# Optimization experiments

Hardware: AMD Instinct MI355X
Metric: run time of the kernel (lower is better)

## Reference

```python
import jax, jax.numpy as jnp
import numpy as np

NEG_INF = -1e9  # finite stand-in for Constants.NEG_INF to keep softmax NaN-free


def setup_inputs() -> dict:
    key = jax.random.key(0)
    ks = jax.random.split(key, 6)
    B, Lq, Lk, D = 32, 1024, 1024, 1024
    query = jax.random.normal(ks[0], (B, Lq, D), dtype=jnp.float32)
    context = jax.random.normal(ks[1], (B, Lk, D), dtype=jnp.float32)
    ql = jax.random.randint(ks[2], (B,), 1, Lq + 1).astype(jnp.int32)
    cl = jax.random.randint(ks[3], (B,), 1, Lk + 1).astype(jnp.int32)
    # pad_packed_sequence pads to the max length in batch -> force max present
    ql = ql.at[0].set(Lq)
    cl = cl.at[0].set(Lk)
    W_in = jax.random.normal(ks[4], (D, D), dtype=jnp.float32) * (D ** -0.5)
    W_out = jax.random.normal(ks[5], (D, 2 * D), dtype=jnp.float32) * ((2 * D) ** -0.5)
    return {"query": query, "context": context, "query_lengths": ql,
            "context_lengths": cl, "W_in": W_in, "W_out": W_out}


def reference(query, context, query_lengths, context_lengths, W_in, W_out):
    B, Lq, D = query.shape
    Lk = context.shape[1]
    # attention_type == 'general': project queries
    q = jnp.einsum('bqd,ed->bqe', query, W_in)                      # [B,Lq,D]
    scores = jnp.einsum('bqd,bkd->bqk', q, context)                 # [B,Lq,Lk]
    # pack/pad round-trips == length mask on both query and context axes
    qmask = jnp.arange(Lq)[None, :] < query_lengths[:, None]        # [B,Lq]
    kmask = jnp.arange(Lk)[None, :] < context_lengths[:, None]      # [B,Lk]
    mask = qmask[:, :, None] & kmask[:, None, :]                    # [B,Lq,Lk]
    scores_m = jnp.where(mask, scores, NEG_INF)
    weights = jax.nn.softmax(scores_m, axis=2)
    mix = jnp.einsum('bqk,bkd->bqd', weights, context)              # [B,Lq,D]
    combined = jnp.concatenate([mix, q], axis=2)                    # [B,Lq,2D]
    output = jnp.tanh(jnp.einsum('bqc,dc->bqd', combined, W_out))   # [B,Lq,D]
    return output, scores_m
```

## Files before the change

kernel.cpp:

```cpp
#include <hip/hip_runtime.h>
#include <math.h>

#define BM 128
#define BN 128
#define BK 32
#define KP 40

typedef __bf16 bf16x8 __attribute__((ext_vector_type(8)));
typedef float  floatx4 __attribute__((ext_vector_type(4)));

__device__ __forceinline__ unsigned short f2bf(float x) {
    unsigned int u = __float_as_uint(x);
    u += 0x7FFFu + ((u >> 16) & 1u);
    return (unsigned short)(u >> 16);
}
__device__ __forceinline__ float bf2f(unsigned short h) {
    return __uint_as_float(((unsigned int)h) << 16);
}

template <bool LO>
__device__ __forceinline__ void cvt_store(unsigned short* H, unsigned short* L,
                                          int idx, float4 v) {
    unsigned short h0 = f2bf(v.x), h1 = f2bf(v.y), h2 = f2bf(v.z), h3 = f2bf(v.w);
    *(ushort4*)(H + idx) = make_ushort4(h0, h1, h2, h3);
    if (LO) {
        unsigned short l0 = f2bf(v.x - bf2f(h0)), l1 = f2bf(v.y - bf2f(h1));
        unsigned short l2 = f2bf(v.z - bf2f(h2)), l3 = f2bf(v.w - bf2f(h3));
        *(ushort4*)(L + idx) = make_ushort4(l0, l1, l2, l3);
    }
}

template <int EPI, bool SOFTA, bool SPLITA, bool TRANSB, int NPASS>
__global__ __launch_bounds__(256, 2) void mfma_gemm(
    const float* __restrict__ A, const float* __restrict__ A2,
    const float* __restrict__ B, float* __restrict__ C,
    int K, int lda, int ldb, int ldc,
    long long aBatch, long long bBatch, long long cBatch,
    const float2* __restrict__ stats, long long statsBatch,
    const int* __restrict__ qlen, const int* __restrict__ klen)
{
    constexpr bool PIPE = (NPASS == 1);

    const int b = blockIdx.z;
    A += aBatch * b;
    B += bBatch * b;
    C += cBatch * b;

    __shared__ __align__(16) unsigned short smem[(BM + BN) * KP * 2];
    unsigned short* Ah = smem;
    unsigned short* Al = Ah + BM * KP;
    unsigned short* Bh = Al + BM * KP;
    unsigned short* Bl = Bh + BN * KP;
    float* Bt = (float*)Bh;

    const int tid = threadIdx.x;
    const int m0 = blockIdx.y * BM;
    const int n0 = blockIdx.x * BN;

    const int sr = tid >> 3;
    const int sc = (tid & 7) << 2;

    const int wv = tid >> 6;
    const int wm = (wv >> 1) << 6;
    const int wn = (wv & 1) << 6;
    const int lane = tid & 63;
    const int lm = lane & 15;
    const int lk = (lane >> 4) << 3;

    floatx4 acc[4][4];
#pragma unroll
    for (int i = 0; i < 4; i++)
#pragma unroll
        for (int j = 0; j < 4; j++) acc[i][j] = (floatx4)0.f;

    float2 st[4];
    if (SOFTA) {
        const float2* sp = stats + statsBatch * b;
#pragma unroll
        for (int r = 0; r < 4; r++) st[r] = sp[m0 + (r << 5) + sr];
    }

    auto ldA = [&](int k0, float4* va) {
        const float* Ap = A;
        int kk = k0;
        if (SPLITA) {
            const int half = K >> 1;
            Ap = (k0 < half) ? A : A2;
            kk = k0 & (half - 1);
        }
#pragma unroll
        for (int r = 0; r < 4; r++) {
            const int row = (r << 5) + sr;
            va[r] = *(const float4*)(Ap + (size_t)(m0 + row) * lda + kk + sc);
        }
    };
    auto ldB = [&](int k0, float4* vb) {
        if (!TRANSB) {
#pragma unroll
            for (int r = 0; r < 4; r++) {
                const int row = (r << 5) + sr;
                vb[r] = *(const float4*)(B + (size_t)(n0 + row) * ldb + k0 + sc);
            }
        } else {
            const int kr = tid >> 3;
            const int c4 = (tid & 7) << 2;
#pragma unroll
            for (int r = 0; r < 4; r++) {
                const int col = (r << 5) + c4;
                const float* src = B + (size_t)(k0 + kr) * ldb + n0 + col;
                float2 v0 = *(const float2*)(src);
                float2 v1 = *(const float2*)(src + 2);
                vb[r] = make_float4(v0.x, v0.y, v1.x, v1.y);
            }
        }
    };
    auto stA = [&](const float4* va) {
#pragma unroll
        for (int r = 0; r < 4; r++) {
            float4 v = va[r];
            if (SOFTA) {
                v.x = expf(v.x - st[r].x) * st[r].y;
                v.y = expf(v.y - st[r].x) * st[r].y;
                v.z = expf(v.z - st[r].x) * st[r].y;
                v.w = expf(v.w - st[r].x) * st[r].y;
            }
            cvt_store<NPASS == 3>(Ah, Al, ((r << 5) + sr) * KP + sc, v);
        }
    };
    auto stB = [&](const float4* vb) {
        if (!TRANSB) {
#pragma unroll
            for (int r = 0; r < 4; r++)
                cvt_store<NPASS == 3>(Bh, Bl, ((r << 5) + sr) * KP + sc, vb[r]);
        } else {
            const int kr = tid >> 3;
            const int c4 = (tid & 7) << 2;
#pragma unroll
            for (int r = 0; r < 4; r++) {
                const int col = (r << 5) + c4;
                *(float2*)(Bt + kr * 130 + col)     = make_float2(vb[r].x, vb[r].y);
                *(float2*)(Bt + kr * 130 + col + 2) = make_float2(vb[r].z, vb[r].w);
            }
        }
    };

    float4 va[4], vb[4];
    if (PIPE) { ldA(0, va); ldB(0, vb); }

    for (int k0 = 0; k0 < K; k0 += BK) {
        if (!PIPE) { ldA(k0, va); ldB(k0, vb); }
        stA(va);
        stB(vb);
        __syncthreads();

        if (PIPE && k0 + BK < K) { ldA(k0 + BK, va); ldB(k0 + BK, vb); }

        bf16x8 ah[4], al[4], bh[4], bl[4];
#pragma unroll
        for (int t = 0; t < 4; t++) {
            const int ar = (wm + (t << 4) + lm) * KP + lk;
            ah[t] = *(const bf16x8*)(Ah + ar);
            if constexpr (NPASS == 3) al[t] = *(const bf16x8*)(Al + ar);
        }
        if (!TRANSB) {
#pragma unroll
            for (int t = 0; t < 4; t++) {
                const int br = (wn + (t << 4) + lm) * KP + lk;
                bh[t] = *(const bf16x8*)(Bh + br);
                if constexpr (NPASS == 3) bl[t] = *(const bf16x8*)(Bl + br);
            }
        } else {
#pragma unroll
            for (int t = 0; t < 4; t++) {
                const int n = wn + (t << 4) + lm;
                union { unsigned short u[8]; bf16x8 v; } th, tl;
#pragma unroll
                for (int j = 0; j < 8; j++) {
                    float x = Bt[(lk + j) * 130 + n];
                    unsigned short h = f2bf(x);
                    th.u[j] = h;
                    if constexpr (NPASS == 3) tl.u[j] = f2bf(x - bf2f(h));
                }
                bh[t] = th.v;
                if constexpr (NPASS == 3) bl[t] = tl.v;
            }
        }

#pragma unroll
        for (int i = 0; i < 4; i++)
#pragma unroll
            for (int j = 0; j < 4; j++) {
                if constexpr (NPASS == 3) {
                    acc[i][j] = __builtin_amdgcn_mfma_f32_16x16x32_bf16(al[i], bh[j], acc[i][j], 0, 0, 0);
                    acc[i][j] = __builtin_amdgcn_mfma_f32_16x16x32_bf16(ah[i], bl[j], acc[i][j], 0, 0, 0);
                }
                acc[i][j] = __builtin_amdgcn_mfma_f32_16x16x32_bf16(ah[i], bh[j], acc[i][j], 0, 0, 0);
            }
        __syncthreads();
    }

    int qb = 0, kb = 0;
    if (EPI == 1) { qb = qlen[b]; kb = klen[b]; }
    const int qd = (lane >> 4) << 2;
#pragma unroll
    for (int i = 0; i < 4; i++)
#pragma unroll
        for (int j = 0; j < 4; j++) {
            const int col = n0 + wn + (j << 4) + lm;
#pragma unroll
            for (int r = 0; r < 4; r++) {
                const int row = m0 + wm + (i << 4) + qd + r;
                float v = acc[i][j][r];
                if (EPI == 1) v = (row < qb && col < kb) ? v : -1e9f;
                else if (EPI == 2) v = tanhf(v);
                C[(size_t)row * ldc + col] = v;
            }
        }
}

__global__ __launch_bounds__(256) void row_stats_kernel(
    const float* __restrict__ S, float2* __restrict__ stats, int L)
{
    const int row = blockIdx.x * 4 + (threadIdx.x >> 6);
    const int lane = threadIdx.x & 63;
    const float* p = S + (size_t)row * L;

    float mx = -1e30f;
    for (int j = lane; j < L; j += 64) mx = fmaxf(mx, p[j]);
#pragma unroll
    for (int off = 32; off > 0; off >>= 1) mx = fmaxf(mx, __shfl_xor(mx, off, 64));

    float sm = 0.f;
    for (int j = lane; j < L; j += 64) sm += expf(p[j] - mx);
#pragma unroll
    for (int off = 32; off > 0; off >>= 1) sm += __shfl_xor(sm, off, 64);

    if (lane == 0) stats[row] = make_float2(mx, 1.f / sm);
}

extern "C" void kernel_launch(void* const* d_in, const int* in_sizes, int n_in,
                              void* d_out, int out_size, void* d_ws, size_t ws_size,
                              hipStream_t stream)
{
    const float* query   = (const float*)d_in[0];
    const float* context = (const float*)d_in[1];
    const int*   qlens   = (const int*)d_in[2];
    const int*   clens   = (const int*)d_in[3];
    const float* W_in    = (const float*)d_in[4];
    const float* W_out   = (const float*)d_in[5];

    const int B = 32, Lq = 1024, Lk = 1024, D = 1024;
    const long long nQ = (long long)B * Lq * D;

    float* out    = (float*)d_out;
    float* scores = out + nQ;

    float*  q     = (float*)d_ws;
    float*  mix   = q + nQ;
    float2* stats = (float2*)(mix + nQ);

    mfma_gemm<0, false, false, false, 3><<<dim3(D / BN, (B * Lq) / BM, 1), 256, 0, stream>>>(
        query, nullptr, W_in, q, D, D, D, D,
        0LL, 0LL, 0LL, nullptr, 0LL, nullptr, nullptr);

    mfma_gemm<1, false, false, false, 3><<<dim3(Lk / BN, Lq / BM, B), 256, 0, stream>>>(
        q, nullptr, context, scores, D, D, D, Lk,
        (long long)Lq * D, (long long)Lk * D, (long long)Lq * Lk,
        nullptr, 0LL, qlens, clens);

    row_stats_kernel<<<(B * Lq) / 4, 256, 0, stream>>>(scores, stats, Lk);

    mfma_gemm<0, true, false, true, 1><<<dim3(D / BN, Lq / BM, B), 256, 0, stream>>>(
        scores, nullptr, context, mix, Lk, Lk, D, D,
        (long long)Lq * Lk, (long long)Lk * D, (long long)Lq * D,
        stats, (long long)Lq, nullptr, nullptr);

    mfma_gemm<2, false, true, false, 1><<<dim3(D / BN, (B * Lq) / BM, 1), 256, 0, stream>>>(
        mix, q, W_out, out, 2 * D, D, 2 * D, D,
        0LL, 0LL, 0LL, nullptr, 0LL, nullptr, nullptr);
}
```

Baseline: 1.524 ms.

## Store intermediates and weights as pre-split bf16 planes, transpose-convert B into LDS

```diff
diff --git a/kernel.cpp b/kernel.cpp
--- a/kernel.cpp
+++ b/kernel.cpp
@@ -8,50 +8,56 @@
 
 typedef __bf16 bf16x8 __attribute__((ext_vector_type(8)));
 typedef float  floatx4 __attribute__((ext_vector_type(4)));
-
-__device__ __forceinline__ unsigned short f2bf(float x) {
+typedef unsigned short u16;
+
+__device__ __forceinline__ u16 f2bf(float x) {
     unsigned int u = __float_as_uint(x);
     u += 0x7FFFu + ((u >> 16) & 1u);
-    return (unsigned short)(u >> 16);
-}
-__device__ __forceinline__ float bf2f(unsigned short h) {
+    return (u16)(u >> 16);
+}
+__device__ __forceinline__ float bf2f(u16 h) {
     return __uint_as_float(((unsigned int)h) << 16);
 }
 
 template <bool LO>
-__device__ __forceinline__ void cvt_store(unsigned short* H, unsigned short* L,
-                                          int idx, float4 v) {
-    unsigned short h0 = f2bf(v.x), h1 = f2bf(v.y), h2 = f2bf(v.z), h3 = f2bf(v.w);
+__device__ __forceinline__ void cvt_store(u16* H, u16* L, int idx, float4 v) {
+    u16 h0 = f2bf(v.x), h1 = f2bf(v.y), h2 = f2bf(v.z), h3 = f2bf(v.w);
     *(ushort4*)(H + idx) = make_ushort4(h0, h1, h2, h3);
     if (LO) {
-        unsigned short l0 = f2bf(v.x - bf2f(h0)), l1 = f2bf(v.y - bf2f(h1));
-        unsigned short l2 = f2bf(v.z - bf2f(h2)), l3 = f2bf(v.w - bf2f(h3));
+        u16 l0 = f2bf(v.x - bf2f(h0)), l1 = f2bf(v.y - bf2f(h1));
+        u16 l2 = f2bf(v.z - bf2f(h2)), l3 = f2bf(v.w - bf2f(h3));
         *(ushort4*)(L + idx) = make_ushort4(l0, l1, l2, l3);
     }
 }
 
-template <int EPI, bool SOFTA, bool SPLITA, bool TRANSB, int NPASS>
+enum OpMode { OP_F32 = 0, OP_PLANES = 1, OP_BF16 = 2 };
+
+template <int EPI, bool SOFTA, bool SPLITA, bool TRANSB, int NPASS, int AMODE, int BMODE>
 __global__ __launch_bounds__(256, 2) void mfma_gemm(
-    const float* __restrict__ A, const float* __restrict__ A2,
-    const float* __restrict__ B, float* __restrict__ C,
+    const void* __restrict__ Av, const void* __restrict__ A2v,
+    const void* __restrict__ Bv, const void* __restrict__ B2v,
+    void* __restrict__ Cv, void* __restrict__ C2v,
     int K, int lda, int ldb, int ldc,
     long long aBatch, long long bBatch, long long cBatch,
     const float2* __restrict__ stats, long long statsBatch,
     const int* __restrict__ qlen, const int* __restrict__ klen)
 {
-    constexpr bool PIPE = (NPASS == 1);
-
     const int b = blockIdx.z;
-    A += aBatch * b;
-    B += bBatch * b;
-    C += cBatch * b;
-
-    __shared__ __align__(16) unsigned short smem[(BM + BN) * KP * 2];
-    unsigned short* Ah = smem;
-    unsigned short* Al = Ah + BM * KP;
-    unsigned short* Bh = Al + BM * KP;
-    unsigned short* Bl = Bh + BN * KP;
-    float* Bt = (float*)Bh;
+
+    const float* A_f  = (const float*)Av + aBatch * b;
+    const u16*   A_h  = (const u16*)Av + aBatch * b;
+    const u16*   A_l  = (const u16*)A2v + aBatch * b;
+    const u16*   A2_h = (const u16*)A2v;
+    const float* B_f  = (const float*)Bv + bBatch * b;
+    const u16*   B_h  = (const u16*)Bv + bBatch * b;
+    const u16*   B_l  = (const u16*)B2v + bBatch * b;
+
+    constexpr int LP = (NPASS == 3) ? 2 : 1;
+    __shared__ __align__(16) u16 smem[(BM + BN) * KP * LP];
+    u16* Ah = smem;
+    u16* Al = Ah + (NPASS == 3 ? BM * KP : 0);
+    u16* Bh = Ah + BM * KP * LP;
+    u16* Bl = Bh + (NPASS == 3 ? BN * KP : 0);
 
     const int tid = threadIdx.x;
     const int m0 = blockIdx.y * BM;
@@ -80,80 +86,132 @@
         for (int r = 0; r < 4; r++) st[r] = sp[m0 + (r << 5) + sr];
     }
 
-    auto ldA = [&](int k0, float4* va) {
-        const float* Ap = A;
-        int kk = k0;
-        if (SPLITA) {
-            const int half = K >> 1;
-            Ap = (k0 < half) ? A : A2;
-            kk = k0 & (half - 1);
-        }
-#pragma unroll
-        for (int r = 0; r < 4; r++) {
-            const int row = (r << 5) + sr;
-            va[r] = *(const float4*)(Ap + (size_t)(m0 + row) * lda + kk + sc);
+    float4  vaf[4]; ushort4 vah[4], vaL[4];
+    float4  vbf[4]; ushort4 vbh[4], vbL[4];
+
+    auto ldA = [&](int k0) {
+        if constexpr (AMODE == OP_F32) {
+#pragma unroll
+            for (int r = 0; r < 4; r++) {
+                const int row = (r << 5) + sr;
+                vaf[r] = *(const float4*)(A_f + (size_t)(m0 + row) * lda + k0 + sc);
+            }
+        } else if constexpr (AMODE == OP_PLANES) {
+#pragma unroll
+            for (int r = 0; r < 4; r++) {
+                const int row = (r << 5) + sr;
+                const size_t off = (size_t)(m0 + row) * lda + k0 + sc;
+                vah[r] = *(const ushort4*)(A_h + off);
+                vaL[r] = *(const ushort4*)(A_l + off);
+            }
+        } else {
+            const u16* Ap = A_h;
+            int kk = k0;
+            if constexpr (SPLITA) {
+                const int half = K >> 1;
+                Ap = (k0 < half) ? A_h : A2_h;
+                kk = k0 & (half - 1);
+            }
+#pragma unroll
+            for (int r = 0; r < 4; r++) {
+                const int row = (r << 5) + sr;
+                vah[r] = *(const ushort4*)(Ap + (size_t)(m0 + row) * lda + kk + sc);
+            }
         }
     };
-    auto ldB = [&](int k0, float4* vb) {
-        if (!TRANSB) {
-#pragma unroll
-            for (int r = 0; r < 4; r++) {
-                const int row = (r << 5) + sr;
-                vb[r] = *(const float4*)(B + (size_t)(n0 + row) * ldb + k0 + sc);
-            }
-        } else {
+    auto ldB = [&](int k0) {
+        if constexpr (TRANSB) {
             const int kr = tid >> 3;
             const int c4 = (tid & 7) << 2;
 #pragma unroll
             for (int r = 0; r < 4; r++) {
                 const int col = (r << 5) + c4;
-                const float* src = B + (size_t)(k0 + kr) * ldb + n0 + col;
+                const float* src = B_f + (size_t)(k0 + kr) * ldb + n0 + col;
                 float2 v0 = *(const float2*)(src);
                 float2 v1 = *(const float2*)(src + 2);
-                vb[r] = make_float4(v0.x, v0.y, v1.x, v1.y);
+                vbf[r] = make_float4(v0.x, v0.y, v1.x, v1.y);
+            }
+        } else if constexpr (BMODE == OP_F32) {
+#pragma unroll
+            for (int r = 0; r < 4; r++) {
+                const int row = (r << 5) + sr;
+                vbf[r] = *(const float4*)(B_f + (size_t)(n0 + row) * ldb + k0 + sc);
+            }
+        } else if constexpr (BMODE == OP_PLANES) {
+#pragma unroll
+            for (int r = 0; r < 4; r++) {
+                const int row = (r << 5) + sr;
+                const size_t off = (size_t)(n0 + row) * ldb + k0 + sc;
+                vbh[r] = *(const ushort4*)(B_h + off);
+                vbL[r] = *(const ushort4*)(B_l + off);
+            }
+        } else {
+#pragma unroll
+            for (int r = 0; r < 4; r++) {
+                const int row = (r << 5) + sr;
+                vbh[r] = *(const ushort4*)(B_h + (size_t)(n0 + row) * ldb + k0 + sc);
             }
         }
     };
-    auto stA = [&](const float4* va) {
+    auto stA = [&]() {
 #pragma unroll
         for (int r = 0; r < 4; r++) {
-            float4 v = va[r];
-            if (SOFTA) {
-                v.x = expf(v.x - st[r].x) * st[r].y;
-                v.y = expf(v.y - st[r].x) * st[r].y;
-                v.z = expf(v.z - st[r].x) * st[r].y;
-                v.w = expf(v.w - st[r].x) * st[r].y;
-            }
-            cvt_store<NPASS == 3>(Ah, Al, ((r << 5) + sr) * KP + sc, v);
+            const int idx = ((r << 5) + sr) * KP + sc;
+            if constexpr (AMODE == OP_F32) {
+                float4 v = vaf[r];
+                if (SOFTA) {
+                    v.x = expf(v.x - st[r].x) * st[r].y;
+                    v.y = expf(v.y - st[r].x) * st[r].y;
+                    v.z = expf(v.z - st[r].x) * st[r].y;
+                    v.w = expf(v.w - st[r].x) * st[r].y;
+                }
+                cvt_store<NPASS == 3>(Ah, Al, idx, v);
+            } else if constexpr (AMODE == OP_PLANES) {
+                *(ushort4*)(Ah + idx) = vah[r];
+                *(ushort4*)(Al + idx) = vaL[r];
+            } else {
+                *(ushort4*)(Ah + idx) = vah[r];
+            }
         }
     };
-    auto stB = [&](const float4* vb) {
-        if (!TRANSB) {
-#pragma unroll
-            for (int r = 0; r < 4; r++)
-                cvt_store<NPASS == 3>(Bh, Bl, ((r << 5) + sr) * KP + sc, vb[r]);
-        } else {
+    auto stB = [&]() {
+        if constexpr (TRANSB) {
             const int kr = tid >> 3;
             const int c4 = (tid & 7) << 2;
 #pragma unroll
             for (int r = 0; r < 4; r++) {
                 const int col = (r << 5) + c4;
-                *(float2*)(Bt + kr * 130 + col)     = make_float2(vb[r].x, vb[r].y);
-                *(float2*)(Bt + kr * 130 + col + 2) = make_float2(vb[r].z, vb[r].w);
+                const float4 v = vbf[r];
+                Bh[(col + 0) * KP + kr] = f2bf(v.x);
+                Bh[(col + 1) * KP + kr] = f2bf(v.y);
+                Bh[(col + 2) * KP + kr] = f2bf(v.z);
+                Bh[(col + 3) * KP + kr] = f2bf(v.w);
+            }
+        } else {
+#pragma unroll
+            for (int r = 0; r < 4; r++) {
+                const int idx = ((r << 5) + sr) * KP + sc;
+                if constexpr (BMODE == OP_F32) {
+                    cvt_store<NPASS == 3>(Bh, Bl, idx, vbf[r]);
+                } else if constexpr (BMODE == OP_PLANES) {
+                    *(ushort4*)(Bh + idx) = vbh[r];
+                    *(ushort4*)(Bl + idx) = vbL[r];
+                } else {
+                    *(ushort4*)(Bh + idx) = vbh[r];
+                }
             }
         }
     };
 
-    float4 va[4], vb[4];
-    if (PIPE) { ldA(0, va); ldB(0, vb); }
+    ldA(0);
+    ldB(0);
 
     for (int k0 = 0; k0 < K; k0 += BK) {
-        if (!PIPE) { ldA(k0, va); ldB(k0, vb); }
-        stA(va);
-        stB(vb);
+        stA();
+        stB();
         __syncthreads();
 
-        if (PIPE && k0 + BK < K) { ldA(k0 + BK, va); ldB(k0 + BK, vb); }
+        if (k0 + BK < K) { ldA(k0 + BK); ldB(k0 + BK); }
 
         bf16x8 ah[4], al[4], bh[4], bl[4];
 #pragma unroll
@@ -162,28 +220,11 @@
             ah[t] = *(const bf16x8*)(Ah + ar);
             if constexpr (NPASS == 3) al[t] = *(const bf16x8*)(Al + ar);
         }
-        if (!TRANSB) {
-#pragma unroll
-            for (int t = 0; t < 4; t++) {
-                const int br = (wn + (t << 4) + lm) * KP + lk;
-                bh[t] = *(const bf16x8*)(Bh + br);
-                if constexpr (NPASS == 3) bl[t] = *(const bf16x8*)(Bl + br);
-            }
-        } else {
-#pragma unroll
-            for (int t = 0; t < 4; t++) {
-                const int n = wn + (t << 4) + lm;
-                union { unsigned short u[8]; bf16x8 v; } th, tl;
-#pragma unroll
-                for (int j = 0; j < 8; j++) {
-                    float x = Bt[(lk + j) * 130 + n];
-                    unsigned short h = f2bf(x);
-                    th.u[j] = h;
-                    if constexpr (NPASS == 3) tl.u[j] = f2bf(x - bf2f(h));
-                }
-                bh[t] = th.v;
-                if constexpr (NPASS == 3) bl[t] = tl.v;
-            }
+#pragma unroll
+        for (int t = 0; t < 4; t++) {
+            const int br = (wn + (t << 4) + lm) * KP + lk;
+            bh[t] = *(const bf16x8*)(Bh + br);
+            if constexpr (NPASS == 3) bl[t] = *(const bf16x8*)(Bl + br);
         }
 
 #pragma unroll
@@ -199,6 +240,9 @@
         __syncthreads();
     }
 
+    float* C_f = (float*)Cv + cBatch * b;
+    u16*   C_h = (u16*)Cv + cBatch * b;
+    u16*   C_l = (u16*)C2v + cBatch * b;
     int qb = 0, kb = 0;
     if (EPI == 1) { qb = qlen[b]; kb = klen[b]; }
     const int qd = (lane >> 4) << 2;
@@ -210,10 +254,21 @@
 #pragma unroll
             for (int r = 0; r < 4; r++) {
                 const int row = m0 + wm + (i << 4) + qd + r;
+                const size_t off = (size_t)row * ldc + col;
                 float v = acc[i][j][r];
-                if (EPI == 1) v = (row < qb && col < kb) ? v : -1e9f;
-                else if (EPI == 2) v = tanhf(v);
-                C[(size_t)row * ldc + col] = v;
+                if constexpr (EPI == 0) {
+                    C_f[off] = v;
+                } else if constexpr (EPI == 1) {
+                    C_f[off] = (row < qb && col < kb) ? v : -1e9f;
+                } else if constexpr (EPI == 2) {
+                    C_f[off] = tanhf(v);
+                } else if constexpr (EPI == 3) {
+                    const u16 h = f2bf(v);
+                    C_h[off] = h;
+                    C_l[off] = f2bf(v - bf2f(h));
+                } else {
+                    C_h[off] = f2bf(v);
+                }
             }
         }
 }
@@ -236,6 +291,28 @@
     for (int off = 32; off > 0; off >>= 1) sm += __shfl_xor(sm, off, 64);
 
     if (lane == 0) stats[row] = make_float2(mx, 1.f / sm);
+}
+
+__global__ __launch_bounds__(256) void cvt_hilo_kernel(
+    const float* __restrict__ s, u16* __restrict__ hi, u16* __restrict__ lo, int n4)
+{
+    const int stride = gridDim.x * 256;
+    for (int i = blockIdx.x * 256 + threadIdx.x; i < n4; i += stride) {
+        float4 v = ((const float4*)s)[i];
+        u16 h0 = f2bf(v.x), h1 = f2bf(v.y), h2 = f2bf(v.z), h3 = f2bf(v.w);
+        ((ushort4*)hi)[i] = make_ushort4(h0, h1, h2, h3);
+        ((ushort4*)lo)[i] = make_ushort4(f2bf(v.x - bf2f(h0)), f2bf(v.y - bf2f(h1)),
+                                         f2bf(v.z - bf2f(h2)), f2bf(v.w - bf2f(h3)));
+    }
+}
+__global__ __launch_bounds__(256) void cvt_bf16_kernel(
+    const float* __restrict__ s, u16* __restrict__ d, int n4)
+{
+    const int stride = gridDim.x * 256;
+    for (int i = blockIdx.x * 256 + threadIdx.x; i < n4; i += stride) {
+        float4 v = ((const float4*)s)[i];
+        ((ushort4*)d)[i] = make_ushort4(f2bf(v.x), f2bf(v.y), f2bf(v.z), f2bf(v.w));
+    }
 }
 
 extern "C" void kernel_launch(void* const* d_in, const int* in_sizes, int n_in,
@@ -255,27 +332,38 @@
     float* out    = (float*)d_out;
     float* scores = out + nQ;
 
-    float*  q     = (float*)d_ws;
-    float*  mix   = q + nQ;
-    float2* stats = (float2*)(mix + nQ);
-
-    mfma_gemm<0, false, false, false, 3><<<dim3(D / BN, (B * Lq) / BM, 1), 256, 0, stream>>>(
-        query, nullptr, W_in, q, D, D, D, D,
-        0LL, 0LL, 0LL, nullptr, 0LL, nullptr, nullptr);
-
-    mfma_gemm<1, false, false, false, 3><<<dim3(Lk / BN, Lq / BM, B), 256, 0, stream>>>(
-        q, nullptr, context, scores, D, D, D, Lk,
-        (long long)Lq * D, (long long)Lk * D, (long long)Lq * Lk,
+    u16* q_hi    = (u16*)d_ws;
+    u16* q_lo    = q_hi + nQ;
+    u16* mixb    = q_lo + nQ;
+    u16* w_in_hi = mixb + nQ;
+    u16* w_in_lo = w_in_hi + (1 << 20);
+    u16* w_out_b = w_in_lo + (1 << 20);
+    float2* stats = (float2*)(w_out_b + (2 << 20));
+
+    cvt_hilo_kernel<<<1024, 256, 0, stream>>>(W_in, w_in_hi, w_in_lo, (D * D) / 4);
+    cvt_bf16_kernel<<<2048, 256, 0, stream>>>(W_out, w_out_b, (D * 2 * D) / 4);
+
+    mfma_gemm<3, false, false, false, 3, OP_F32, OP_PLANES>
+        <<<dim3(D / BN, (B * Lq) / BM, 1), 256, 0, stream>>>(
+        query, nullptr, w_in_hi, w_in_lo, q_hi, q_lo,
+        D, D, D, D, 0LL, 0LL, 0LL, nullptr, 0LL, nullptr, nullptr);
+
+    mfma_gemm<1, false, false, false, 3, OP_PLANES, OP_F32>
+        <<<dim3(Lk / BN, Lq / BM, B), 256, 0, stream>>>(
+        q_hi, q_lo, context, nullptr, scores, nullptr,
+        D, D, D, Lk, (long long)Lq * D, (long long)Lk * D, (long long)Lq * Lk,
         nullptr, 0LL, qlens, clens);
 
     row_stats_kernel<<<(B * Lq) / 4, 256, 0, stream>>>(scores, stats, Lk);
 
-    mfma_gemm<0, true, false, true, 1><<<dim3(D / BN, Lq / BM, B), 256, 0, stream>>>(
-        scores, nullptr, context, mix, Lk, Lk, D, D,
-        (long long)Lq * Lk, (long long)Lk * D, (long long)Lq * D,
+    mfma_gemm<4, true, false, true, 1, OP_F32, OP_F32>
+        <<<dim3(D / BN, Lq / BM, B), 256, 0, stream>>>(
+        scores, nullptr, context, nullptr, mixb, nullptr,
+        Lk, Lk, D, D, (long long)Lq * Lk, (long long)Lk * D, (long long)Lq * D,
         stats, (long long)Lq, nullptr, nullptr);
 
-    mfma_gemm<2, false, true, false, 1><<<dim3(D / BN, (B * Lq) / BM, 1), 256, 0, stream>>>(
-        mix, q, W_out, out, 2 * D, D, 2 * D, D,
-        0LL, 0LL, 0LL, nullptr, 0LL, nullptr, nullptr);
-}
+    mfma_gemm<2, false, true, false, 1, OP_BF16, OP_BF16>
+        <<<dim3(D / BN, (B * Lq) / BM, 1), 256, 0, stream>>>(
+        mixb, q_hi, w_out_b, nullptr, out, nullptr,
+        2 * D, D, 2 * D, D, 0LL, 0LL, 0LL, nullptr, 0LL, nullptr, nullptr);
+}
```

Result: faster. 1.385 ms (-9.1%).
